# Performance work log

Hardware: AMD Instinct MI355X
Metric: run time of the kernel (lower is better)

Reference implementation:

```python
import jax, jax.numpy as jnp
import numpy as np

B = 524288      # batch
D = 16          # ds_dim
N = 32          # number of dynamical systems
H = 128         # gating hidden width


def setup_inputs() -> dict:
    key = jax.random.key(0)
    ks = jax.random.split(key, 8)
    x_cur = jax.random.normal(ks[0], (B, D), dtype=jnp.float32)
    W1 = jax.random.normal(ks[1], (H, D), dtype=jnp.float32) * 0.1
    b1 = jax.random.normal(ks[2], (H,), dtype=jnp.float32) * 0.1
    W2 = jax.random.normal(ks[3], (N, H), dtype=jnp.float32) * 0.1
    b2 = jax.random.normal(ks[4], (N,), dtype=jnp.float32) * 0.1
    # B matrices are PSD (geotorch.positive_semidefinite), C are skew-symmetric (geotorch.skew)
    Braw = jax.random.normal(ks[5], (N, D, D), dtype=jnp.float32) * 0.3
    B_mats = jnp.einsum('nij,nkj->nik', Braw, Braw)  # PSD: R R^T
    Craw = jax.random.normal(ks[6], (N, D, D), dtype=jnp.float32) * 0.3
    C_mats = 0.5 * (Craw - jnp.swapaxes(Craw, -1, -2))  # skew-symmetric
    x_target = jax.random.normal(ks[7], (1, D), dtype=jnp.float32)
    return {"x_cur": x_cur, "W1": W1, "b1": b1, "W2": W2, "b2": b2,
            "B_mats": B_mats, "C_mats": C_mats, "x_target": x_target}


def reference(x_cur, W1, b1, W2, b2, B_mats, C_mats, x_target):
    # gating weights: softmax(Linear -> ReLU -> Linear)
    h = jax.nn.relu(x_cur @ W1.T + b1)          # [B, H]
    w_all = jax.nn.softmax(h @ W2.T + b2, axis=1)  # [B, N]
    # per-system linear map A_i = B_i + C_i applied to (x* - x)
    A = B_mats + C_mats                          # [N, D, D]
    diff = x_target - x_cur                      # [B, D]
    # torch.mm(A, diff.T).T == diff @ A.T -> proj[b,n,k] = sum_d A[n,k,d] diff[b,d]
    proj = jnp.einsum('nkd,bd->bnk', A, diff)    # [B, N, D]
    out = jnp.einsum('bn,bnk->bk', w_all, proj)  # [B, D]
    return out
```

## Files before the change

### kernel.cpp

```cpp
#include <hip/hip_runtime.h>

#define BATCH 524288

typedef __bf16 bf16x8 __attribute__((ext_vector_type(8)));
typedef __bf16 bf16x2 __attribute__((ext_vector_type(2)));
typedef float f32x4 __attribute__((ext_vector_type(4)));
typedef float f32x8 __attribute__((ext_vector_type(8)));
typedef float f32x2 __attribute__((ext_vector_type(2)));

#define SMEM_BYTES (20512 + 4 * 4352)

__device__ __forceinline__ f32x8 load8(const float* __restrict__ p) {
    float4 a = *(const float4*)p;
    float4 b = *(const float4*)(p + 4);
    f32x8 v = {a.x, a.y, a.z, a.w, b.x, b.y, b.z, b.w};
    return v;
}

__device__ __forceinline__ int pack2bf(float a, float b) {
    f32x2 v = {a, b};
    bf16x2 p = __builtin_convertvector(v, bf16x2);
    return __builtin_bit_cast(int, p);
}

__global__ __launch_bounds__(256, 4) void andp_v5(
    const float* __restrict__ x_cur,
    const float* __restrict__ W1,
    const float* __restrict__ b1,
    const float* __restrict__ W2,
    const float* __restrict__ b2,
    const float* __restrict__ Bm,
    const float* __restrict__ Cm,
    const float* __restrict__ x_t,
    float* __restrict__ out)
{
    extern __shared__ char smem[];
    int* sA2i = (int*)smem;
    int* sW1i = (int*)(smem + 16384);
    const int tid = threadIdx.x;

#pragma unroll
    for (int i = 0; i < 16; ++i) {
        int o2 = tid + i * 256;
        int o  = o2 * 2;
        int kk = o >> 9, k = (o >> 5) & 15, qp = (o >> 3) & 3, j = o & 7;
        int n = 2 * kk + (qp >> 1), d = (qp & 1) * 8 + j;
        int src = n * 256 + k * 16 + d;
        float2 bv = *(const float2*)(Bm + src);
        float2 cv = *(const float2*)(Cm + src);
        sA2i[o2] = pack2bf(bv.x + cv.x, bv.y + cv.y);
    }
#pragma unroll
    for (int i = 0; i < 4; ++i) {
        int p0 = tid + i * 256;
        float2 v = *(const float2*)(W1 + 2 * p0);
        sW1i[p0] = pack2bf(v.x, v.y);
    }
    if (tid < 8) sW1i[1024 + tid] = 0;

    const int wave = tid >> 6, lane = tid & 63;
    const int c = lane & 15, q = lane >> 4;
    const int qh = q >> 1;
    const int hh = (q & 1) * 8;
    const int tflip = qh & 1;
    const int qx2 = q ^ (2 * ((c >> 3) & 1));
    const int c4 = c * 4;
    const int sh = qh ? 0 : 16;

    const char* sW1f = smem + 16384;
    const int w1base = (q < 2) ? (c * 32 + q * 16) : 4096;
    const int w1step = (q < 2) ? 512 : 0;
    __bf16* hsw = (__bf16*)(smem + 20512 + wave * 4352);

    bf16x8 w2f[2][4];
#pragma unroll
    for (int t2 = 0; t2 < 2; ++t2)
#pragma unroll
        for (int kk = 0; kk < 4; ++kk)
            w2f[t2][kk] = __builtin_convertvector(
                load8(W2 + (t2 * 16 + c) * 128 + kk * 32 + q * 8), bf16x8);
    float b1v[8];
#pragma unroll
    for (int t = 0; t < 8; ++t) b1v[t] = b1[t * 16 + c];
    float b2v[2][4];
#pragma unroll
    for (int t2 = 0; t2 < 2; ++t2)
#pragma unroll
        for (int r = 0; r < 4; ++r) b2v[t2][r] = b2[t2 * 16 + q * 4 + r];
    const f32x8 xtv = load8(x_t + hh);

    __syncthreads();

    const int blk_row = blockIdx.x * 256 + wave * 64;
    const f32x4 z4 = {0.f, 0.f, 0.f, 0.f};

#pragma unroll 1
    for (int p = 0; p < 2; ++p) {
        const int r0 = blk_row + p * 32;

        bf16x8 af[2];
        f32x8 dif[2];
#pragma unroll
        for (int t01 = 0; t01 < 2; ++t01) {
            f32x8 xv = load8(x_cur + (size_t)(r0 + t01 * 16 + c) * 16 + hh);
            af[t01]  = __builtin_convertvector(xv, bf16x8);
            dif[t01] = xtv - xv;
        }

        int wpk[2][4];

#pragma unroll
        for (int t01 = 0; t01 < 2; ++t01) {
#pragma unroll
            for (int th = 0; th < 2; ++th) {
                f32x4 acc1[4];
#pragma unroll
                for (int t4 = 0; t4 < 4; ++t4) {
                    int t = th * 4 + t4;
                    bf16x8 w1b = *(const bf16x8*)(sW1f + w1base + t * w1step);
                    acc1[t4] = __builtin_amdgcn_mfma_f32_16x16x32_bf16(af[t01], w1b, z4, 0, 0, 0);
                }
#pragma unroll
                for (int t4 = 0; t4 < 4; ++t4) {
                    int t = th * 4 + t4;
                    const int colb = (t ^ tflip) * 16 + c;
#pragma unroll
                    for (int r = 0; r < 4; ++r) {
                        float v = fmaxf(acc1[t4][r] + b1v[t], 0.f);
                        hsw[(q * 4 + r) * 136 + colb] = (__bf16)v;
                    }
                }
            }

            f32x4 acc2[2];
            acc2[0] = z4; acc2[1] = z4;
#pragma unroll
            for (int kk = 0; kk < 4; ++kk) {
                bf16x8 hb = *(const bf16x8*)(hsw + c * 136 + kk * 32 + qx2 * 8);
                acc2[0] = __builtin_amdgcn_mfma_f32_16x16x32_bf16(w2f[0][kk], hb, acc2[0], 0, 0, 0);
                acc2[1] = __builtin_amdgcn_mfma_f32_16x16x32_bf16(w2f[1][kk], hb, acc2[1], 0, 0, 0);
            }

            float l[8];
#pragma unroll
            for (int t2 = 0; t2 < 2; ++t2)
#pragma unroll
                for (int r = 0; r < 4; ++r) l[t2 * 4 + r] = acc2[t2][r] + b2v[t2][r];
            float mx = l[0];
#pragma unroll
            for (int i = 1; i < 8; ++i) mx = fmaxf(mx, l[i]);
            mx = fmaxf(mx, __shfl_xor(mx, 16, 64));
            mx = fmaxf(mx, __shfl_xor(mx, 32, 64));
            float e[8], s = 0.f;
#pragma unroll
            for (int i = 0; i < 8; ++i) { e[i] = __expf(l[i] - mx); s += e[i]; }
            s += __shfl_xor(s, 16, 64);
            s += __shfl_xor(s, 32, 64);
            float inv = 1.0f / s;
#pragma unroll
            for (int t2 = 0; t2 < 2; ++t2)
#pragma unroll
                for (int rp = 0; rp < 2; ++rp)
                    wpk[t01][t2 * 2 + rp] =
                        pack2bf(e[t2 * 4 + 2 * rp] * inv, e[t2 * 4 + 2 * rp + 1] * inv);
        }

        f32x4 acc3[2];
        acc3[0] = z4; acc3[1] = z4;
#pragma unroll
        for (int kk = 0; kk < 16; ++kk) {
            const int widx = (kk >> 3) * 2 + (kk & 1);
            const int bpi = c4 + ((kk >> 1) & 3) * 64;
            int bp0 = __builtin_amdgcn_ds_bpermute(bpi, wpk[0][widx]);
            int bp1 = __builtin_amdgcn_ds_bpermute(bpi, wpk[1][widx]);
            float w0 = __builtin_bit_cast(float, (unsigned)(bp0 << sh) & 0xffff0000u);
            float w1 = __builtin_bit_cast(float, (unsigned)(bp1 << sh) & 0xffff0000u);
            bf16x8 a2f = *(const bf16x8*)(smem + kk * 1024 + (c * 4 + q) * 16);
            bf16x8 g0 = __builtin_convertvector(dif[0] * w0, bf16x8);
            bf16x8 g1 = __builtin_convertvector(dif[1] * w1, bf16x8);
            acc3[0] = __builtin_amdgcn_mfma_f32_16x16x32_bf16(a2f, g0, acc3[0], 0, 0, 0);
            acc3[1] = __builtin_amdgcn_mfma_f32_16x16x32_bf16(a2f, g1, acc3[1], 0, 0, 0);
        }

#pragma unroll
        for (int t01 = 0; t01 < 2; ++t01) {
            float4 st = make_float4(acc3[t01][0], acc3[t01][1], acc3[t01][2], acc3[t01][3]);
            *(float4*)(out + (size_t)(r0 + t01 * 16 + c) * 16 + q * 4) = st;
        }
    }
}

extern "C" void kernel_launch(void* const* d_in, const int* in_sizes, int n_in,
                              void* d_out, int out_size, void* d_ws, size_t ws_size,
                              hipStream_t stream) {
    const float* x_cur = (const float*)d_in[0];
    const float* W1    = (const float*)d_in[1];
    const float* b1    = (const float*)d_in[2];
    const float* W2    = (const float*)d_in[3];
    const float* b2    = (const float*)d_in[4];
    const float* Bm    = (const float*)d_in[5];
    const float* Cm    = (const float*)d_in[6];
    const float* x_t   = (const float*)d_in[7];
    float* out = (float*)d_out;

    const int blocks = BATCH / 256;
    andp_v5<<<blocks, 256, SMEM_BYTES, stream>>>(
        x_cur, W1, b1, W2, b2, Bm, Cm, x_t, out);
}
```

Baseline: 136.1 us.

## Interleave hidden-layer chunks with second GEMM and drop softmax max-subtraction

```diff
diff --git a/kernel.cpp b/kernel.cpp
--- a/kernel.cpp
+++ b/kernel.cpp
@@ -8,7 +8,7 @@
 typedef float f32x8 __attribute__((ext_vector_type(8)));
 typedef float f32x2 __attribute__((ext_vector_type(2)));
 
-#define SMEM_BYTES (20512 + 4 * 4352)
+#define SMEM_BYTES (28704 + 4 * 1088)
 
 __device__ __forceinline__ f32x8 load8(const float* __restrict__ p) {
     float4 a = *(const float4*)p;
@@ -23,7 +23,7 @@
     return __builtin_bit_cast(int, p);
 }
 
-__global__ __launch_bounds__(256, 4) void andp_v5(
+__global__ __launch_bounds__(256, 4) void andp_v6(
     const float* __restrict__ x_cur,
     const float* __restrict__ W1,
     const float* __restrict__ b1,
@@ -37,6 +37,7 @@
     extern __shared__ char smem[];
     int* sA2i = (int*)smem;
     int* sW1i = (int*)(smem + 16384);
+    int* sW2i = (int*)(smem + 20512);
     const int tid = threadIdx.x;
 
 #pragma unroll
@@ -57,28 +58,31 @@
         sW1i[p0] = pack2bf(v.x, v.y);
     }
     if (tid < 8) sW1i[1024 + tid] = 0;
+#pragma unroll
+    for (int i = 0; i < 8; ++i) {
+        int o2 = tid + i * 256;
+        int chunk = o2 >> 8, r = o2 & 255;
+        int ln = r >> 2, j2 = r & 3;
+        int q = ln >> 4, cc = ln & 15;
+        int t2 = chunk >> 2, kk = chunk & 3;
+        int src = (t2 * 16 + cc) * 128 + kk * 32 + q * 8 + j2 * 2;
+        float2 v = *(const float2*)(W2 + src);
+        sW2i[o2] = pack2bf(v.x, v.y);
+    }
 
     const int wave = tid >> 6, lane = tid & 63;
     const int c = lane & 15, q = lane >> 4;
     const int qh = q >> 1;
     const int hh = (q & 1) * 8;
-    const int tflip = qh & 1;
-    const int qx2 = q ^ (2 * ((c >> 3) & 1));
     const int c4 = c * 4;
     const int sh = qh ? 0 : 16;
 
     const char* sW1f = smem + 16384;
     const int w1base = (q < 2) ? (c * 32 + q * 16) : 4096;
     const int w1step = (q < 2) ? 512 : 0;
-    __bf16* hsw = (__bf16*)(smem + 20512 + wave * 4352);
-
-    bf16x8 w2f[2][4];
-#pragma unroll
-    for (int t2 = 0; t2 < 2; ++t2)
-#pragma unroll
-        for (int kk = 0; kk < 4; ++kk)
-            w2f[t2][kk] = __builtin_convertvector(
-                load8(W2 + (t2 * 16 + c) * 128 + kk * 32 + q * 8), bf16x8);
+    const char* sW2f = smem + 20512 + lane * 16;
+    __bf16* hcw = (__bf16*)(smem + 28704 + wave * 1088);
+
     float b1v[8];
 #pragma unroll
     for (int t = 0; t < 8; ++t) b1v[t] = b1[t * 16 + c];
@@ -111,49 +115,36 @@
 
 #pragma unroll
         for (int t01 = 0; t01 < 2; ++t01) {
-#pragma unroll
-            for (int th = 0; th < 2; ++th) {
-                f32x4 acc1[4];
-#pragma unroll
-                for (int t4 = 0; t4 < 4; ++t4) {
-                    int t = th * 4 + t4;
-                    bf16x8 w1b = *(const bf16x8*)(sW1f + w1base + t * w1step);
-                    acc1[t4] = __builtin_amdgcn_mfma_f32_16x16x32_bf16(af[t01], w1b, z4, 0, 0, 0);
-                }
-#pragma unroll
-                for (int t4 = 0; t4 < 4; ++t4) {
-                    int t = th * 4 + t4;
-                    const int colb = (t ^ tflip) * 16 + c;
-#pragma unroll
-                    for (int r = 0; r < 4; ++r) {
-                        float v = fmaxf(acc1[t4][r] + b1v[t], 0.f);
-                        hsw[(q * 4 + r) * 136 + colb] = (__bf16)v;
-                    }
-                }
-            }
-
             f32x4 acc2[2];
             acc2[0] = z4; acc2[1] = z4;
 #pragma unroll
-            for (int kk = 0; kk < 4; ++kk) {
-                bf16x8 hb = *(const bf16x8*)(hsw + c * 136 + kk * 32 + qx2 * 8);
-                acc2[0] = __builtin_amdgcn_mfma_f32_16x16x32_bf16(w2f[0][kk], hb, acc2[0], 0, 0, 0);
-                acc2[1] = __builtin_amdgcn_mfma_f32_16x16x32_bf16(w2f[1][kk], hb, acc2[1], 0, 0, 0);
+            for (int th = 0; th < 4; ++th) {
+                bf16x8 w1a = *(const bf16x8*)(sW1f + w1base + (2 * th) * w1step);
+                bf16x8 w1b = *(const bf16x8*)(sW1f + w1base + (2 * th + 1) * w1step);
+                f32x4 a1a = __builtin_amdgcn_mfma_f32_16x16x32_bf16(af[t01], w1a, z4, 0, 0, 0);
+                f32x4 a1b = __builtin_amdgcn_mfma_f32_16x16x32_bf16(af[t01], w1b, z4, 0, 0, 0);
+#pragma unroll
+                for (int r = 0; r < 4; ++r) {
+                    float va = fmaxf(a1a[r] + b1v[2 * th], 0.f);
+                    float vb = fmaxf(a1b[r] + b1v[2 * th + 1], 0.f);
+                    hcw[(q * 4 + r) * 34 + c]      = (__bf16)va;
+                    hcw[(q * 4 + r) * 34 + 16 + c] = (__bf16)vb;
+                }
+                bf16x8 hb = *(const bf16x8*)(hcw + c * 34 + q * 8);
+                bf16x8 w20 = *(const bf16x8*)(sW2f + (0 * 4 + th) * 1024);
+                bf16x8 w21 = *(const bf16x8*)(sW2f + (1 * 4 + th) * 1024);
+                acc2[0] = __builtin_amdgcn_mfma_f32_16x16x32_bf16(w20, hb, acc2[0], 0, 0, 0);
+                acc2[1] = __builtin_amdgcn_mfma_f32_16x16x32_bf16(w21, hb, acc2[1], 0, 0, 0);
             }
 
-            float l[8];
+            float e[8], s = 0.f;
 #pragma unroll
             for (int t2 = 0; t2 < 2; ++t2)
 #pragma unroll
-                for (int r = 0; r < 4; ++r) l[t2 * 4 + r] = acc2[t2][r] + b2v[t2][r];
-            float mx = l[0];
-#pragma unroll
-            for (int i = 1; i < 8; ++i) mx = fmaxf(mx, l[i]);
-            mx = fmaxf(mx, __shfl_xor(mx, 16, 64));
-            mx = fmaxf(mx, __shfl_xor(mx, 32, 64));
-            float e[8], s = 0.f;
-#pragma unroll
-            for (int i = 0; i < 8; ++i) { e[i] = __expf(l[i] - mx); s += e[i]; }
+                for (int r = 0; r < 4; ++r) {
+                    e[t2 * 4 + r] = __expf(acc2[t2][r] + b2v[t2][r]);
+                    s += e[t2 * 4 + r];
+                }
             s += __shfl_xor(s, 16, 64);
             s += __shfl_xor(s, 32, 64);
             float inv = 1.0f / s;
@@ -204,6 +195,6 @@
     float* out = (float*)d_out;
 
     const int blocks = BATCH / 256;
-    andp_v5<<<blocks, 256, SMEM_BYTES, stream>>>(
+    andp_v6<<<blocks, 256, SMEM_BYTES, stream>>>(
         x_cur, W1, b1, W2, b2, Bm, Cm, x_t, out);
 }
```

Result: faster. 131.1 us (-3.6%).
